# Performance work log

Measured on AMD Instinct MI355X. Metric: run time of the kernel, lower is better.

## Reference

```python
import jax, jax.numpy as jnp
import numpy as np

N = 50000      # nodes
E = 500000     # edges (before self-loops)
D_IN = 128     # embedding_dim
C = 256        # intermediate_dim (per-head out channels)
H = 1          # heads
SLOPE = 0.2    # LeakyReLU negative slope (PyG default)


def setup_inputs() -> dict:
    key = jax.random.key(0)
    ks = jax.random.split(key, 8)
    x = jax.random.normal(ks[0], (N, D_IN), dtype=jnp.float32)
    edge_index = jax.random.randint(ks[1], (2, E), 0, N, dtype=jnp.int32)
    W1 = jax.random.normal(ks[2], (H * C, D_IN), dtype=jnp.float32) / np.sqrt(D_IN)
    a1_src = jax.random.normal(ks[3], (H, C), dtype=jnp.float32) / np.sqrt(C)
    a1_dst = jax.random.normal(ks[4], (H, C), dtype=jnp.float32) / np.sqrt(C)
    b1 = jnp.zeros((C,), dtype=jnp.float32)
    W2 = jax.random.normal(ks[5], (H * C, C), dtype=jnp.float32) / np.sqrt(C)
    a2_src = jax.random.normal(ks[6], (H, C), dtype=jnp.float32) / np.sqrt(C)
    a2_dst = jax.random.normal(ks[7], (H, C), dtype=jnp.float32) / np.sqrt(C)
    b2 = jnp.zeros((C,), dtype=jnp.float32)
    return dict(x=x, edge_index=edge_index, W1=W1, a1_src=a1_src, a1_dst=a1_dst,
                b1=b1, W2=W2, a2_src=a2_src, a2_dst=a2_dst, b2=b2)


def gat_conv(x, src, dst, W, a_src, a_dst, b):
    # x: [N, Din]; W: [H*C, Din]; a_*: [H, C]; b: [C]
    h = (x @ W.T).reshape(N, H, C)                      # [N, H, C]
    e_src = jnp.einsum('nhc,hc->nh', h, a_src)          # [N, H]
    e_dst = jnp.einsum('nhc,hc->nh', h, a_dst)          # [N, H]
    e = jax.nn.leaky_relu(e_src[src] + e_dst[dst], SLOPE)  # [Etot, H]
    # segment softmax over destination nodes (self-loops guarantee >=1 edge per node)
    m = jax.lax.stop_gradient(jax.ops.segment_max(e, dst, num_segments=N))
    p = jnp.exp(e - m[dst])                             # [Etot, H]
    denom = jax.ops.segment_sum(p, dst, num_segments=N)  # [N, H]
    alpha = p / (denom[dst] + 1e-16)                    # [Etot, H]
    out = jax.ops.segment_sum(h[src] * alpha[:, :, None], dst, num_segments=N)  # [N, H, C]
    return out.mean(axis=1) + b                         # concat=False -> head mean; [N, C]


def reference(x, edge_index, W1, a1_src, a1_dst, b1, W2, a2_src, a2_dst, b2):
    # PyG GATConv default add_self_loops=True
    loop = jnp.arange(N, dtype=edge_index.dtype)
    src = jnp.concatenate([edge_index[0], loop])
    dst = jnp.concatenate([edge_index[1], loop])
    x1 = jax.nn.relu(gat_conv(x, src, dst, W1, a1_src, a1_dst, b1))
    x2 = jax.nn.relu(gat_conv(x1, src, dst, W2, a2_src, a2_dst, b2))
    return jnp.concatenate([x1, x2], axis=-1)           # [N, 2*C]
```

## Files before the change

kernel.cpp:

```cpp
#include <hip/hip_runtime.h>
#include <hip/hip_bf16.h>
#include <math.h>

#define NNODES 50000
#define NEDGES 500000
#define ETOT   (NEDGES + NNODES)
#define DIN    128
#define CH     256
#define SLOPE  0.2f

#define SCAN_TILE 1024
#define NSCAN ((NNODES + SCAN_TILE - 1) / SCAN_TILE)

typedef __attribute__((ext_vector_type(8))) short short8;
typedef __attribute__((ext_vector_type(4))) float f32x4;

static __device__ __forceinline__ float wave_reduce_max(float v) {
#pragma unroll
  for (int off = 32; off > 0; off >>= 1) v = fmaxf(v, __shfl_xor(v, off));
  return v;
}
static __device__ __forceinline__ float wave_reduce_sum(float v) {
#pragma unroll
  for (int off = 32; off > 0; off >>= 1) v += __shfl_xor(v, off);
  return v;
}

static __device__ __forceinline__ unsigned short f2bf(float f) {
  unsigned int u = __float_as_uint(f);
  unsigned int r = (u + 0x7fffu + ((u >> 16) & 1u)) >> 16;
  return (unsigned short)r;
}
static __device__ __forceinline__ float bf2f(unsigned short u) {
  return __uint_as_float(((unsigned int)u) << 16);
}

#define W1N4 (CH * DIN / 4)
#define W2N4 (CH * CH / 4)
__global__ __launch_bounds__(256) void init_and_cast(
    int* __restrict__ deg,
    float* __restrict__ eS1, float* __restrict__ eD1,
    float* __restrict__ eS2, float* __restrict__ eD2,
    const float* __restrict__ W1, const float* __restrict__ W2,
    unsigned short* __restrict__ Wb1, unsigned short* __restrict__ Wb2) {
  int i = blockIdx.x * 256 + threadIdx.x;
  if (i < NNODES) {
    deg[i] = 0;
    eS1[i] = 0.f; eD1[i] = 0.f;
    eS2[i] = 0.f; eD2[i] = 0.f;
  }
  if (i < W1N4 + W2N4) {
    const float* src;
    unsigned short* dst;
    int j;
    if (i < W1N4) { src = W1; dst = Wb1; j = i; }
    else          { src = W2; dst = Wb2; j = i - W1N4; }
    float4 v = *(const float4*)(src + (size_t)j * 4);
    ushort4 o;
    o.x = f2bf(v.x); o.y = f2bf(v.y); o.z = f2bf(v.z); o.w = f2bf(v.w);
    *(ushort4*)(dst + (size_t)j * 4) = o;
  }
}

__global__ __launch_bounds__(256) void scan_blocksums(const int* __restrict__ deg,
                                                      int* __restrict__ bsums) {
  __shared__ int sdata[4];
  int b = blockIdx.x;
  int tid = threadIdx.x;
  int idx = b * SCAN_TILE + tid * 4;
  int s = 0;
  if (idx + 3 < NNODES) {
    int4 v = *(const int4*)(deg + idx);
    s = v.x + v.y + v.z + v.w;
  } else {
#pragma unroll
    for (int j = 0; j < 4; j++) if (idx + j < NNODES) s += deg[idx + j];
  }
#pragma unroll
  for (int off = 32; off > 0; off >>= 1) s += __shfl_xor(s, off);
  if ((tid & 63) == 0) sdata[tid >> 6] = s;
  __syncthreads();
  if (tid == 0) bsums[b] = sdata[0] + sdata[1] + sdata[2] + sdata[3];
}

__global__ __launch_bounds__(64) void scan_bsums(const int* __restrict__ bsums,
                                                 int* __restrict__ boffs,
                                                 int* __restrict__ rowptr) {
  int tid = threadIdx.x;
  int v = (tid < NSCAN) ? bsums[tid] : 0;
  int x = v;
#pragma unroll
  for (int off = 1; off < 64; off <<= 1) {
    int t = __shfl_up(x, off);
    if (tid >= off) x += t;
  }
  if (tid < NSCAN) boffs[tid] = x - v;
  if (tid == 63) rowptr[NNODES] = x;
}

__global__ __launch_bounds__(256) void scan_final(const int* __restrict__ deg,
                                                  const int* __restrict__ boffs,
                                                  int* __restrict__ rowptr,
                                                  int* __restrict__ cursor) {
  __shared__ int wsums[4];
  int b = blockIdx.x;
  int tid = threadIdx.x;
  int lane = tid & 63;
  int base = b * SCAN_TILE + tid * 4;
  int d[4];
  int s = 0;
#pragma unroll
  for (int j = 0; j < 4; j++) {
    d[j] = (base + j < NNODES) ? deg[base + j] : 0;
    s += d[j];
  }
  int x = s;
#pragma unroll
  for (int off = 1; off < 64; off <<= 1) {
    int t = __shfl_up(x, off);
    if (lane >= off) x += t;
  }
  if (lane == 63) wsums[tid >> 6] = x;
  __syncthreads();
  int woff = 0;
  int w = tid >> 6;
  for (int i = 0; i < w; i++) woff += wsums[i];
  int excl = boffs[b] + woff + (x - s);
#pragma unroll
  for (int j = 0; j < 4; j++) {
    if (base + j < NNODES) { rowptr[base + j] = excl; cursor[base + j] = excl; }
    excl += d[j];
  }
}

__global__ void scatter_kernel(const int* __restrict__ ei, int* __restrict__ cursor,
                               int* __restrict__ csr_src) {
  int e = blockIdx.x * blockDim.x + threadIdx.x;
  if (e >= ETOT) return;
  int src, dst;
  if (e < NEDGES) { src = ei[e]; dst = ei[NEDGES + e]; }
  else            { src = e - NEDGES; dst = src; }
  int slot = atomicAdd(&cursor[dst], 1);
  csr_src[slot] = src;
}

#define TM 128
#define TN 128
#define TK 64
#define LDA (TK + 8)
#define LDC (TN + 8)
#define GEMM_GRID (2 * ((NNODES + TM - 1) / TM))
#define DEG_BLOCKS ((ETOT + 255) / 256)

static __device__ __forceinline__ void gemm_body(
    const float* __restrict__ Xf, const unsigned short* __restrict__ Xb, int ldx,
    const unsigned short* __restrict__ W, int K,
    unsigned short* __restrict__ Hout, int M,
    const float* __restrict__ a_src, const float* __restrict__ a_dst,
    float* __restrict__ eS, float* __restrict__ eD,
    int bm, int bn) {
  __shared__ short smem[TM * LDA * 2];
  short* As = smem;
  short* Bs = smem + TM * LDA;
  short* Cs = smem;
  int tid = threadIdx.x;
  int wid = tid >> 6;
  int lane = tid & 63;
  int wm = (wid & 1) * 64;
  int wn = (wid >> 1) * 64;
  int lrow = lane & 15;
  int lk8 = (lane >> 4) * 8;

  int srow = tid >> 3;
  int skoff = (tid & 7) * 8;

  f32x4 acc[4][4] = {};

  for (int k0 = 0; k0 < K; k0 += TK) {
#pragma unroll
    for (int i = 0; i < 4; i++) {
      int r = srow + 32 * i;
      int gm = bm + r;
      short8 v = {};
      if (gm < M) {
        if (Xf) {
          const float* p = Xf + (size_t)gm * ldx + k0 + skoff;
          float4 f0 = *(const float4*)(p);
          float4 f1 = *(const float4*)(p + 4);
          v[0] = (short)f2bf(f0.x); v[1] = (short)f2bf(f0.y);
          v[2] = (short)f2bf(f0.z); v[3] = (short)f2bf(f0.w);
          v[4] = (short)f2bf(f1.x); v[5] = (short)f2bf(f1.y);
          v[6] = (short)f2bf(f1.z); v[7] = (short)f2bf(f1.w);
        } else {
          v = *(const short8*)(Xb + (size_t)gm * ldx + k0 + skoff);
        }
      }
      *(short8*)(&As[r * LDA + skoff]) = v;
      short8 w = *(const short8*)(W + (size_t)(bn + r) * K + k0 + skoff);
      *(short8*)(&Bs[r * LDA + skoff]) = w;
    }
    __syncthreads();
#pragma unroll
    for (int kk = 0; kk < TK; kk += 32) {
      short8 a[4], b[4];
#pragma unroll
      for (int mi = 0; mi < 4; mi++)
        a[mi] = *(const short8*)(&As[(wm + mi * 16 + lrow) * LDA + kk + lk8]);
#pragma unroll
      for (int ni = 0; ni < 4; ni++)
        b[ni] = *(const short8*)(&Bs[(wn + ni * 16 + lrow) * LDA + kk + lk8]);
#pragma unroll
      for (int mi = 0; mi < 4; mi++)
#pragma unroll
        for (int ni = 0; ni < 4; ni++)
          acc[mi][ni] = __builtin_amdgcn_mfma_f32_16x16x32_bf16(a[mi], b[ni], acc[mi][ni], 0, 0, 0);
    }
    __syncthreads();
  }

  int crow = (lane >> 4) * 4;
  int ccol = lane & 15;

  float asv[4], adv[4];
#pragma unroll
  for (int ni = 0; ni < 4; ni++) {
    int c = bn + wn + ni * 16 + ccol;
    asv[ni] = a_src[c];
    adv[ni] = a_dst[c];
  }
#pragma unroll
  for (int mi = 0; mi < 4; mi++) {
#pragma unroll
    for (int r = 0; r < 4; r++) {
      float s = 0.f, d = 0.f;
#pragma unroll
      for (int ni = 0; ni < 4; ni++) {
        float h = acc[mi][ni][r];
        s += h * asv[ni];
        d += h * adv[ni];
      }
#pragma unroll
      for (int off = 1; off < 16; off <<= 1) {
        s += __shfl_xor(s, off);
        d += __shfl_xor(d, off);
      }
      int gm = bm + wm + mi * 16 + crow + r;
      if (ccol == 0 && gm < M) {
        atomicAdd(&eS[gm], s);
        atomicAdd(&eD[gm], d);
      }
    }
  }

#pragma unroll
  for (int mi = 0; mi < 4; mi++) {
#pragma unroll
    for (int ni = 0; ni < 4; ni++) {
#pragma unroll
      for (int r = 0; r < 4; r++) {
        int row = wm + mi * 16 + crow + r;
        int col = wn + ni * 16 + ccol;
        Cs[row * LDC + col] = (short)f2bf(acc[mi][ni][r]);
      }
    }
  }
  __syncthreads();
  int orow = tid >> 4;
  int ocol = (tid & 15) * 8;
#pragma unroll
  for (int pp = 0; pp < 8; pp++) {
    int row = pp * 16 + orow;
    int gm = bm + row;
    if (gm < M) {
      short8 v = *(const short8*)(&Cs[row * LDC + ocol]);
      *(short8*)(&Hout[(size_t)gm * CH + bn + ocol]) = v;
    }
  }
}

__global__ __launch_bounds__(256) void gemm1_deg(
    const float* __restrict__ Xf, const unsigned short* __restrict__ W,
    unsigned short* __restrict__ Hout,
    const float* __restrict__ a_src, const float* __restrict__ a_dst,
    float* __restrict__ eS, float* __restrict__ eD,
    const int* __restrict__ ei, int* __restrict__ deg) {
  if (blockIdx.x >= GEMM_GRID) {
    int e = (blockIdx.x - GEMM_GRID) * 256 + threadIdx.x;
    if (e < ETOT) {
      int dst = (e < NEDGES) ? ei[NEDGES + e] : (e - NEDGES);
      atomicAdd(&deg[dst], 1);
    }
    return;
  }
  int bn = (blockIdx.x & 1) * TN;
  int bm = (blockIdx.x >> 1) * TM;
  gemm_body(Xf, (const unsigned short*)nullptr, DIN, W, DIN, Hout, NNODES,
            a_src, a_dst, eS, eD, bm, bn);
}

__global__ __launch_bounds__(256) void gemm_l2(
    const unsigned short* __restrict__ Xb, const unsigned short* __restrict__ W,
    unsigned short* __restrict__ Hout,
    const float* __restrict__ a_src, const float* __restrict__ a_dst,
    float* __restrict__ eS, float* __restrict__ eD) {
  int bn = blockIdx.x * TN;
  int bm = blockIdx.y * TM;
  gemm_body((const float*)nullptr, Xb, CH, W, CH, Hout, NNODES,
            a_src, a_dst, eS, eD, bm, bn);
}

__global__ __launch_bounds__(256) void aggregate_kernel(
    const unsigned short* __restrict__ Hmb, const float* __restrict__ eS,
    const float* __restrict__ eD, const int* __restrict__ rowptr,
    const int* __restrict__ csr_src, const float* __restrict__ bias,
    float* __restrict__ out, int outOffset, unsigned short* __restrict__ xout) {
  int n = blockIdx.x * 4 + (threadIdx.x >> 6);
  if (n >= NNODES) return;
  int lane = threadIdx.x & 63;
  int half = lane >> 5;
  int cg = lane & 31;
  int beg = rowptr[n], end = rowptr[n + 1];
  int deg = end - beg;
  float ed = eD[n];

  float acc8[8];
#pragma unroll
  for (int k = 0; k < 8; k++) acc8[k] = 0.f;

  if (deg <= 64) {
    int src = 0;
    float e = -1e30f;
    if (lane < deg) {
      src = csr_src[beg + lane];
      float t = eS[src] + ed;
      e = (t >= 0.f) ? t : SLOPE * t;
    }
    float m = wave_reduce_max(e);
    float p = (lane < deg) ? __expf(e - m) : 0.f;
    float inv = 1.f / (wave_reduce_sum(p) + 1e-16f);
    float av = p * inv;

    for (int j0 = 0; j0 < deg; j0 += 16) {
      uint4 hv[8];
      float al[8];
#pragma unroll
      for (int t = 0; t < 8; t++) {
        int j = j0 + 2 * t + half;
        int jj = (j < deg) ? j : deg - 1;
        int sj = __shfl(src, jj);
        float aj = __shfl(av, jj);
        al[t] = (j < deg) ? aj : 0.f;
        hv[t] = *(const uint4*)(Hmb + (size_t)sj * CH + cg * 8);
      }
#pragma unroll
      for (int t = 0; t < 8; t++) {
        acc8[0] += al[t] * __uint_as_float(hv[t].x << 16);
        acc8[1] += al[t] * __uint_as_float(hv[t].x & 0xffff0000u);
        acc8[2] += al[t] * __uint_as_float(hv[t].y << 16);
        acc8[3] += al[t] * __uint_as_float(hv[t].y & 0xffff0000u);
        acc8[4] += al[t] * __uint_as_float(hv[t].z << 16);
        acc8[5] += al[t] * __uint_as_float(hv[t].z & 0xffff0000u);
        acc8[6] += al[t] * __uint_as_float(hv[t].w << 16);
        acc8[7] += al[t] * __uint_as_float(hv[t].w & 0xffff0000u);
      }
    }
  } else {
    float m = -1e30f;
    for (int i = lane; i < deg; i += 64) {
      float e = eS[csr_src[beg + i]] + ed;
      e = (e >= 0.f) ? e : SLOPE * e;
      m = fmaxf(m, e);
    }
    m = wave_reduce_max(m);
    float ds = 0.f;
    for (int i = lane; i < deg; i += 64) {
      float e = eS[csr_src[beg + i]] + ed;
      e = (e >= 0.f) ? e : SLOPE * e;
      ds += __expf(e - m);
    }
    float inv = 1.f / (wave_reduce_sum(ds) + 1e-16f);
    for (int j = 0; j < deg; j += 2) {
      int jj = j + half;
      int k = beg + ((jj < deg) ? jj : deg - 1);
      int s = csr_src[k];
      float e = eS[s] + ed;
      e = (e >= 0.f) ? e : SLOPE * e;
      float alpha = (jj < deg) ? __expf(e - m) * inv : 0.f;
      uint4 u = *(const uint4*)(Hmb + (size_t)s * CH + cg * 8);
      acc8[0] += alpha * __uint_as_float(u.x << 16);
      acc8[1] += alpha * __uint_as_float(u.x & 0xffff0000u);
      acc8[2] += alpha * __uint_as_float(u.y << 16);
      acc8[3] += alpha * __uint_as_float(u.y & 0xffff0000u);
      acc8[4] += alpha * __uint_as_float(u.z << 16);
      acc8[5] += alpha * __uint_as_float(u.z & 0xffff0000u);
      acc8[6] += alpha * __uint_as_float(u.w << 16);
      acc8[7] += alpha * __uint_as_float(u.w & 0xffff0000u);
    }
  }

#pragma unroll
  for (int k = 0; k < 8; k++) acc8[k] += __shfl_xor(acc8[k], 32);

  float a0 = half ? acc8[4] : acc8[0];
  float a1 = half ? acc8[5] : acc8[1];
  float a2 = half ? acc8[6] : acc8[2];
  float a3 = half ? acc8[7] : acc8[3];
  int cbase = cg * 8 + half * 4;
  float4 b = *(const float4*)(bias + cbase);
  float4 o;
  o.x = fmaxf(a0 + b.x, 0.f);
  o.y = fmaxf(a1 + b.y, 0.f);
  o.z = fmaxf(a2 + b.z, 0.f);
  o.w = fmaxf(a3 + b.w, 0.f);
  *(float4*)(out + (size_t)n * 512 + outOffset + cbase) = o;
  if (xout) {
    ushort4 ob;
    ob.x = f2bf(o.x); ob.y = f2bf(o.y); ob.z = f2bf(o.z); ob.w = f2bf(o.w);
    *(ushort4*)(xout + (size_t)n * CH + cbase) = ob;
  }
}

extern "C" void kernel_launch(void* const* d_in, const int* in_sizes, int n_in,
                              void* d_out, int out_size, void* d_ws, size_t ws_size,
                              hipStream_t stream) {
  const float* x   = (const float*)d_in[0];
  const int*   ei  = (const int*)d_in[1];
  const float* W1  = (const float*)d_in[2];
  const float* a1s = (const float*)d_in[3];
  const float* a1d = (const float*)d_in[4];
  const float* b1  = (const float*)d_in[5];
  const float* W2  = (const float*)d_in[6];
  const float* a2s = (const float*)d_in[7];
  const float* a2d = (const float*)d_in[8];
  const float* b2  = (const float*)d_in[9];
  float* out = (float*)d_out;

  char* ws = (char*)d_ws;
  size_t off = 0;
  auto alloc = [&](size_t bytes) -> void* {
    void* p = ws + off;
    off = (off + bytes + 255) & ~(size_t)255;
    return p;
  };
  unsigned short* Hmb    = (unsigned short*)alloc(sizeof(short) * (size_t)NNODES * CH);
  unsigned short* Xb     = (unsigned short*)alloc(sizeof(short) * (size_t)NNODES * CH);
  unsigned short* Wb1    = (unsigned short*)alloc(sizeof(short) * CH * DIN);
  unsigned short* Wb2    = (unsigned short*)alloc(sizeof(short) * CH * CH);
  float*          eS1    = (float*)alloc(sizeof(float) * NNODES);
  float*          eD1    = (float*)alloc(sizeof(float) * NNODES);
  float*          eS2    = (float*)alloc(sizeof(float) * NNODES);
  float*          eD2    = (float*)alloc(sizeof(float) * NNODES);
  int*            rowptr = (int*)alloc(sizeof(int) * (NNODES + 1));
  int*            cursor = (int*)alloc(sizeof(int) * NNODES);
  int*            csrsrc = (int*)alloc(sizeof(int) * ETOT);
  int*            deg    = (int*)alloc(sizeof(int) * NNODES);
  int*            bsums  = (int*)alloc(sizeof(int) * NSCAN);
  int*            boffs  = (int*)alloc(sizeof(int) * NSCAN);

  int nblk4 = (NNODES + 3) / 4;

  init_and_cast<<<(NNODES + 255) / 256, 256, 0, stream>>>(deg, eS1, eD1, eS2, eD2,
                                                          W1, W2, Wb1, Wb2);

  gemm1_deg<<<GEMM_GRID + DEG_BLOCKS, 256, 0, stream>>>(x, Wb1, Hmb, a1s, a1d,
                                                        eS1, eD1, ei, deg);

  scan_blocksums<<<NSCAN, 256, 0, stream>>>(deg, bsums);
  scan_bsums<<<1, 64, 0, stream>>>(bsums, boffs, rowptr);
  scan_final<<<NSCAN, 256, 0, stream>>>(deg, boffs, rowptr, cursor);
  scatter_kernel<<<(ETOT + 255) / 256, 256, 0, stream>>>(ei, cursor, csrsrc);

  aggregate_kernel<<<nblk4, 256, 0, stream>>>(Hmb, eS1, eD1, rowptr, csrsrc, b1, out, 0, Xb);

  gemm_l2<<<dim3(2, (NNODES + TM - 1) / TM), 256, 0, stream>>>(Xb, Wb2, Hmb, a2s, a2d, eS2, eD2);
  aggregate_kernel<<<nblk4, 256, 0, stream>>>(Hmb, eS2, eD2, rowptr, csrsrc, b2, out, 256,
                                              (unsigned short*)nullptr);
}
```

Measured before the change: 330.2 us.

## Fuse scan and scatter into one kernel; load GEMM tiles directly to LDS

Replaces the three scan kernels and the scatter kernel with a single launch. Scan blocks publish flagged tile sums and look back over predecessors, and scatter blocks spin on a done counter until the scan finishes. This removes several launch gaps but relies on the scan blocks being scheduled before the spinning scatter blocks. The GEMM also uses global_load_lds with an XOR-swizzled unpadded layout for W, and for the bf16 X in layer 2, so the copy skips the register round trip and avoids LDS bank conflicts.

```diff
diff --git a/kernel.cpp b/kernel.cpp
--- a/kernel.cpp
+++ b/kernel.cpp
@@ -11,16 +11,30 @@
 
 #define SCAN_TILE 1024
 #define NSCAN ((NNODES + SCAN_TILE - 1) / SCAN_TILE)
+#define SCAT_BLOCKS ((ETOT + 255) / 256)
+#define FLAGBIT 0x40000000
 
 typedef __attribute__((ext_vector_type(8))) short short8;
 typedef __attribute__((ext_vector_type(4))) float f32x4;
 
+typedef __attribute__((address_space(1))) void gvoid;
+typedef __attribute__((address_space(3))) void lvoid;
+
+static __device__ __forceinline__ void gload_lds16(const void* g, void* l) {
+  __builtin_amdgcn_global_load_lds((const gvoid*)g, (lvoid*)l, 16, 0, 0);
+}
+
 static __device__ __forceinline__ float wave_reduce_max(float v) {
 #pragma unroll
   for (int off = 32; off > 0; off >>= 1) v = fmaxf(v, __shfl_xor(v, off));
   return v;
 }
 static __device__ __forceinline__ float wave_reduce_sum(float v) {
+#pragma unroll
+  for (int off = 32; off > 0; off >>= 1) v += __shfl_xor(v, off);
+  return v;
+}
+static __device__ __forceinline__ int wave_reduce_sum_i(int v) {
 #pragma unroll
   for (int off = 32; off > 0; off >>= 1) v += __shfl_xor(v, off);
   return v;
@@ -42,12 +56,17 @@
     float* __restrict__ eS1, float* __restrict__ eD1,
     float* __restrict__ eS2, float* __restrict__ eD2,
     const float* __restrict__ W1, const float* __restrict__ W2,
-    unsigned short* __restrict__ Wb1, unsigned short* __restrict__ Wb2) {
+    unsigned short* __restrict__ Wb1, unsigned short* __restrict__ Wb2,
+    int* __restrict__ tstate, int* __restrict__ done) {
   int i = blockIdx.x * 256 + threadIdx.x;
   if (i < NNODES) {
     deg[i] = 0;
     eS1[i] = 0.f; eD1[i] = 0.f;
     eS2[i] = 0.f; eD2[i] = 0.f;
+  }
+  if (i <= NSCAN) {
+    if (i < NSCAN) tstate[i] = 0;
+    else           *done = 0;
   }
   if (i < W1N4 + W2N4) {
     const float* src;
@@ -62,49 +81,30 @@
   }
 }
 
-__global__ __launch_bounds__(256) void scan_blocksums(const int* __restrict__ deg,
-                                                      int* __restrict__ bsums) {
-  __shared__ int sdata[4];
+__global__ __launch_bounds__(256) void scan_scatter(
+    const int* __restrict__ deg, int* __restrict__ rowptr, int* __restrict__ cursor,
+    int* __restrict__ tstate, int* __restrict__ done,
+    const int* __restrict__ ei, int* __restrict__ csr_src) {
+  int tid = threadIdx.x;
+  if (blockIdx.x >= NSCAN) {
+    if (tid == 0) {
+      while (__hip_atomic_load(done, __ATOMIC_ACQUIRE, __HIP_MEMORY_SCOPE_AGENT) < NSCAN)
+        __builtin_amdgcn_s_sleep(8);
+    }
+    __syncthreads();
+    int e = (blockIdx.x - NSCAN) * 256 + tid;
+    if (e < ETOT) {
+      int src, dst;
+      if (e < NEDGES) { src = ei[e]; dst = ei[NEDGES + e]; }
+      else            { src = e - NEDGES; dst = src; }
+      int slot = atomicAdd(&cursor[dst], 1);
+      csr_src[slot] = src;
+    }
+    return;
+  }
+  __shared__ int wsums[4];
+  __shared__ int s_boff;
   int b = blockIdx.x;
-  int tid = threadIdx.x;
-  int idx = b * SCAN_TILE + tid * 4;
-  int s = 0;
-  if (idx + 3 < NNODES) {
-    int4 v = *(const int4*)(deg + idx);
-    s = v.x + v.y + v.z + v.w;
-  } else {
-#pragma unroll
-    for (int j = 0; j < 4; j++) if (idx + j < NNODES) s += deg[idx + j];
-  }
-#pragma unroll
-  for (int off = 32; off > 0; off >>= 1) s += __shfl_xor(s, off);
-  if ((tid & 63) == 0) sdata[tid >> 6] = s;
-  __syncthreads();
-  if (tid == 0) bsums[b] = sdata[0] + sdata[1] + sdata[2] + sdata[3];
-}
-
-__global__ __launch_bounds__(64) void scan_bsums(const int* __restrict__ bsums,
-                                                 int* __restrict__ boffs,
-                                                 int* __restrict__ rowptr) {
-  int tid = threadIdx.x;
-  int v = (tid < NSCAN) ? bsums[tid] : 0;
-  int x = v;
-#pragma unroll
-  for (int off = 1; off < 64; off <<= 1) {
-    int t = __shfl_up(x, off);
-    if (tid >= off) x += t;
-  }
-  if (tid < NSCAN) boffs[tid] = x - v;
-  if (tid == 63) rowptr[NNODES] = x;
-}
-
-__global__ __launch_bounds__(256) void scan_final(const int* __restrict__ deg,
-                                                  const int* __restrict__ boffs,
-                                                  int* __restrict__ rowptr,
-                                                  int* __restrict__ cursor) {
-  __shared__ int wsums[4];
-  int b = blockIdx.x;
-  int tid = threadIdx.x;
   int lane = tid & 63;
   int base = b * SCAN_TILE + tid * 4;
   int d[4];
@@ -122,26 +122,37 @@
   }
   if (lane == 63) wsums[tid >> 6] = x;
   __syncthreads();
+  int total = wsums[0] + wsums[1] + wsums[2] + wsums[3];
+  if (tid == 0)
+    __hip_atomic_store(&tstate[b], total | FLAGBIT, __ATOMIC_RELEASE, __HIP_MEMORY_SCOPE_AGENT);
+  if (tid < 64) {
+    int acc = 0;
+    if (lane < b) {
+      int v;
+      do {
+        v = __hip_atomic_load(&tstate[lane], __ATOMIC_ACQUIRE, __HIP_MEMORY_SCOPE_AGENT);
+        if (!(v & FLAGBIT)) __builtin_amdgcn_s_sleep(2);
+      } while (!(v & FLAGBIT));
+      acc = v & ~FLAGBIT;
+    }
+    acc = wave_reduce_sum_i(acc);
+    if (lane == 0) s_boff = acc;
+  }
+  __syncthreads();
+  int boff = s_boff;
   int woff = 0;
   int w = tid >> 6;
   for (int i = 0; i < w; i++) woff += wsums[i];
-  int excl = boffs[b] + woff + (x - s);
+  int excl = boff + woff + (x - s);
 #pragma unroll
   for (int j = 0; j < 4; j++) {
     if (base + j < NNODES) { rowptr[base + j] = excl; cursor[base + j] = excl; }
     excl += d[j];
   }
-}
-
-__global__ void scatter_kernel(const int* __restrict__ ei, int* __restrict__ cursor,
-                               int* __restrict__ csr_src) {
-  int e = blockIdx.x * blockDim.x + threadIdx.x;
-  if (e >= ETOT) return;
-  int src, dst;
-  if (e < NEDGES) { src = ei[e]; dst = ei[NEDGES + e]; }
-  else            { src = e - NEDGES; dst = src; }
-  int slot = atomicAdd(&cursor[dst], 1);
-  csr_src[slot] = src;
+  if (b == NSCAN - 1 && tid == 0) rowptr[NNODES] = boff + total;
+  __syncthreads();
+  if (tid == 0)
+    __hip_atomic_fetch_add(done, 1, __ATOMIC_RELEASE, __HIP_MEMORY_SCOPE_AGENT);
 }
 
 #define TM 128
@@ -149,19 +160,21 @@
 #define TK 64
 #define LDA (TK + 8)
 #define LDC (TN + 8)
+#define SMEM_SHORTS (TM * LDC)
 #define GEMM_GRID (2 * ((NNODES + TM - 1) / TM))
 #define DEG_BLOCKS ((ETOT + 255) / 256)
 
+template <bool XF>
 static __device__ __forceinline__ void gemm_body(
-    const float* __restrict__ Xf, const unsigned short* __restrict__ Xb, int ldx,
+    const float* __restrict__ Xf, const unsigned short* __restrict__ Xb,
     const unsigned short* __restrict__ W, int K,
     unsigned short* __restrict__ Hout, int M,
     const float* __restrict__ a_src, const float* __restrict__ a_dst,
     float* __restrict__ eS, float* __restrict__ eD,
     int bm, int bn) {
-  __shared__ short smem[TM * LDA * 2];
+  __shared__ short smem[SMEM_SHORTS];
   short* As = smem;
-  short* Bs = smem + TM * LDA;
+  short* Bs = smem + (XF ? TM * LDA : TM * TK);
   short* Cs = smem;
   int tid = threadIdx.x;
   int wid = tid >> 6;
@@ -174,41 +187,64 @@
   int srow = tid >> 3;
   int skoff = (tid & 7) * 8;
 
+  int rsub = lane >> 3;
+  int csub = lane & 7;
+  int schunk = (csub ^ rsub) << 3;
+
   f32x4 acc[4][4] = {};
 
   for (int k0 = 0; k0 < K; k0 += TK) {
 #pragma unroll
     for (int i = 0; i < 4; i++) {
-      int r = srow + 32 * i;
-      int gm = bm + r;
-      short8 v = {};
-      if (gm < M) {
-        if (Xf) {
-          const float* p = Xf + (size_t)gm * ldx + k0 + skoff;
+      int R = i * 32 + wid * 8;
+      const unsigned short* g = W + (size_t)(bn + R + rsub) * K + k0 + schunk;
+      gload_lds16(g, &Bs[R * TK]);
+    }
+    if (XF) {
+#pragma unroll
+      for (int i = 0; i < 4; i++) {
+        int r = srow + 32 * i;
+        int gm = bm + r;
+        short8 v = {};
+        if (gm < M) {
+          const float* p = Xf + (size_t)gm * DIN + k0 + skoff;
           float4 f0 = *(const float4*)(p);
           float4 f1 = *(const float4*)(p + 4);
           v[0] = (short)f2bf(f0.x); v[1] = (short)f2bf(f0.y);
           v[2] = (short)f2bf(f0.z); v[3] = (short)f2bf(f0.w);
           v[4] = (short)f2bf(f1.x); v[5] = (short)f2bf(f1.y);
           v[6] = (short)f2bf(f1.z); v[7] = (short)f2bf(f1.w);
-        } else {
-          v = *(const short8*)(Xb + (size_t)gm * ldx + k0 + skoff);
         }
-      }
-      *(short8*)(&As[r * LDA + skoff]) = v;
-      short8 w = *(const short8*)(W + (size_t)(bn + r) * K + k0 + skoff);
-      *(short8*)(&Bs[r * LDA + skoff]) = w;
+        *(short8*)(&As[r * LDA + skoff]) = v;
+      }
+    } else {
+#pragma unroll
+      for (int i = 0; i < 4; i++) {
+        int R = i * 32 + wid * 8;
+        const unsigned short* g = Xb + (size_t)(bm + R + rsub) * K + k0 + schunk;
+        gload_lds16(g, &As[R * TK]);
+      }
     }
     __syncthreads();
 #pragma unroll
     for (int kk = 0; kk < TK; kk += 32) {
       short8 a[4], b[4];
 #pragma unroll
-      for (int mi = 0; mi < 4; mi++)
-        a[mi] = *(const short8*)(&As[(wm + mi * 16 + lrow) * LDA + kk + lk8]);
-#pragma unroll
-      for (int ni = 0; ni < 4; ni++)
-        b[ni] = *(const short8*)(&Bs[(wn + ni * 16 + lrow) * LDA + kk + lk8]);
+      for (int mi = 0; mi < 4; mi++) {
+        int ar = wm + mi * 16 + lrow;
+        if (XF) {
+          a[mi] = *(const short8*)(&As[ar * LDA + kk + lk8]);
+        } else {
+          int ac = (kk + lk8) >> 3;
+          a[mi] = *(const short8*)(&As[ar * TK + ((ac ^ (ar & 7)) << 3)]);
+        }
+      }
+#pragma unroll
+      for (int ni = 0; ni < 4; ni++) {
+        int br = wn + ni * 16 + lrow;
+        int bc = (kk + lk8) >> 3;
+        b[ni] = *(const short8*)(&Bs[br * TK + ((bc ^ (br & 7)) << 3)]);
+      }
 #pragma unroll
       for (int mi = 0; mi < 4; mi++)
 #pragma unroll
@@ -294,8 +330,8 @@
   }
   int bn = (blockIdx.x & 1) * TN;
   int bm = (blockIdx.x >> 1) * TM;
-  gemm_body(Xf, (const unsigned short*)nullptr, DIN, W, DIN, Hout, NNODES,
-            a_src, a_dst, eS, eD, bm, bn);
+  gemm_body<true>(Xf, (const unsigned short*)nullptr, W, DIN, Hout, NNODES,
+                  a_src, a_dst, eS, eD, bm, bn);
 }
 
 __global__ __launch_bounds__(256) void gemm_l2(
@@ -305,8 +341,8 @@
     float* __restrict__ eS, float* __restrict__ eD) {
   int bn = blockIdx.x * TN;
   int bm = blockIdx.y * TM;
-  gemm_body((const float*)nullptr, Xb, CH, W, CH, Hout, NNODES,
-            a_src, a_dst, eS, eD, bm, bn);
+  gemm_body<false>((const float*)nullptr, Xb, W, CH, Hout, NNODES,
+                   a_src, a_dst, eS, eD, bm, bn);
 }
 
 __global__ __launch_bounds__(256) void aggregate_kernel(
@@ -454,25 +490,24 @@
   int*            cursor = (int*)alloc(sizeof(int) * NNODES);
   int*            csrsrc = (int*)alloc(sizeof(int) * ETOT);
   int*            deg    = (int*)alloc(sizeof(int) * NNODES);
-  int*            bsums  = (int*)alloc(sizeof(int) * NSCAN);
-  int*            boffs  = (int*)alloc(sizeof(int) * NSCAN);
+  int*            tstate = (int*)alloc(sizeof(int) * NSCAN);
+  int*            done   = (int*)alloc(sizeof(int));
 
   int nblk4 = (NNODES + 3) / 4;
 
   init_and_cast<<<(NNODES + 255) / 256, 256, 0, stream>>>(deg, eS1, eD1, eS2, eD2,
-                                                          W1, W2, Wb1, Wb2);
+                                                          W1, W2, Wb1, Wb2, tstate, done);
 
   gemm1_deg<<<GEMM_GRID + DEG_BLOCKS, 256, 0, stream>>>(x, Wb1, Hmb, a1s, a1d,
                                                         eS1, eD1, ei, deg);
 
-  scan_blocksums<<<NSCAN, 256, 0, stream>>>(deg, bsums);
-  scan_bsums<<<1, 64, 0, stream>>>(bsums, boffs, rowptr);
-  scan_final<<<NSCAN, 256, 0, stream>>>(deg, boffs, rowptr, cursor);
-  scatter_kernel<<<(ETOT + 255) / 256, 256, 0, stream>>>(ei, cursor, csrsrc);
+  scan_scatter<<<NSCAN + SCAT_BLOCKS, 256, 0, stream>>>(deg, rowptr, cursor,
+                                                        tstate, done, ei, csrsrc);
 
   aggregate_kernel<<<nblk4, 256, 0, stream>>>(Hmb, eS1, eD1, rowptr, csrsrc, b1, out, 0, Xb);
 
   gemm_l2<<<dim3(2, (NNODES + TM - 1) / TM), 256, 0, stream>>>(Xb, Wb2, Hmb, a2s, a2d, eS2, eD2);
+
   aggregate_kernel<<<nblk4, 256, 0, stream>>>(Hmb, eS2, eD2, rowptr, csrsrc, b2, out, 256,
                                               (unsigned short*)nullptr);
 }
```

Measured after the change: 409.9 us. +24.2%, slower.
